# Optimization experiments

Measured on AMD Instinct MI355X. Metric: run time of the kernel, lower is better.

The kernel has to match this reference:

```python
import jax, jax.numpy as jnp
import numpy as np

N = 50000      # nodes
E = 800000     # unique directed edges (avg degree 16)
F = 64         # input_dim
D = 64         # output_dim (== F -> residual is identity)
ALPHA = 0.5
LCS_THR = 0.5  # enable_lcs_masking=True, lcs_threshold=0.5


def setup_inputs() -> dict:
    key = jax.random.key(0)
    ks = jax.random.split(key, 16)
    x = jax.random.normal(ks[0], (N, F), jnp.float32)
    src = jax.random.randint(ks[1], (E,), 0, N, jnp.int32)
    dst = jax.random.randint(ks[2], (E,), 0, N, jnp.int32)
    # integer-valued multiplicities in {1,2,3,4} (recurring-transaction counts)
    counts = jnp.floor(jax.random.uniform(ks[3], (E,), jnp.float32) * 4.0) + 1.0
    def lin(k, fan_in, shape):
        return jax.random.normal(k, shape, jnp.float32) / np.float32(np.sqrt(fan_in))
    return dict(
        x=x, counts=counts,
        W_s2d=lin(ks[4], F, (F, D)), b_s2d=jnp.zeros((D,), jnp.float32),
        W_d2s=lin(ks[5], F, (F, D)), b_d2s=jnp.zeros((D,), jnp.float32),
        W_l1=lin(ks[6], 2 * F, (2 * F, F)), b_l1=jnp.zeros((F,), jnp.float32),
        W_l2=lin(ks[7], F, (F, 1)), b_l2=jnp.zeros((1,), jnp.float32),
        W_g1=lin(ks[8], 2 * D, (2 * D, D)), b_g1=jnp.zeros((D,), jnp.float32),
        W_g2=lin(ks[9], D, (D, 1)), b_g2=jnp.zeros((1,), jnp.float32),
        src=src, dst=dst,
    )


def reference(x, counts, W_s2d, b_s2d, W_d2s, b_d2s,
              W_l1, b_l1, W_l2, b_l2, W_g1, b_g1, W_g2, b_g2,
              src, dst):
    # in/out degrees from full (unmasked) multiplicities, clamped at 1
    in_deg = jnp.maximum(jax.ops.segment_sum(counts, dst, num_segments=N), 1.0)
    out_deg = jnp.maximum(jax.ops.segment_sum(counts, src, num_segments=N), 1.0)

    # LCS per unique edge: sigmoid(MLP([x_src, x_dst])), detached in torch
    lcs_in = jnp.concatenate([x[src], x[dst]], axis=-1)          # [E, 2F]
    lcs = jax.nn.sigmoid(
        jax.nn.relu(lcs_in @ W_l1 + b_l1) @ W_l2 + b_l2)[:, 0]   # [E]
    lcs = jax.lax.stop_gradient(lcs)
    keep = (lcs >= LCS_THR).astype(x.dtype)                      # LCS masking

    # symmetric-normalized edge weights with multiplicity counts
    w = counts * keep * jax.lax.rsqrt(out_deg[src] * in_deg[dst])  # [E]

    # direction-aware message passing (redundancy-eliminated, per unique edge)
    h_s2d = x @ W_s2d + b_s2d                                    # [N, D]
    h_d2s = x @ W_d2s + b_d2s                                    # [N, D]
    m_in = jax.ops.segment_sum(w[:, None] * h_s2d[src], dst, num_segments=N)
    m_out = jax.ops.segment_sum(w[:, None] * h_d2s[dst], src, num_segments=N)

    # node-wise gating over inbound vs outbound flows
    gate = jax.nn.sigmoid(
        jax.nn.relu(jnp.concatenate([m_in, m_out], axis=-1) @ W_g1 + b_g1)
        @ W_g2 + b_g2)                                           # [N, 1]

    # gated alpha-blend + identity residual (input_dim == output_dim)
    out = ALPHA * gate * m_in + (1.0 - ALPHA) * (1.0 - gate) * m_out + x
    return out
```

## Files before the change

### kernel.cpp

```cpp
#include <hip/hip_runtime.h>
#include <math.h>


typedef unsigned long long u64;

#define SLOTS 56

__device__ __forceinline__ float bflo(unsigned u) { return __uint_as_float(u << 16); }
__device__ __forceinline__ float bfhi(unsigned u) { return __uint_as_float(u & 0xffff0000u); }
__device__ __forceinline__ unsigned rne16(float f) {
    unsigned u = __float_as_uint(f);
    return (u + 0x7fffu + ((u >> 16) & 1u)) >> 16;
}

__global__ __launch_bounds__(256, 2) void proj_zero_kernel(
    const float* __restrict__ x,
    const float* __restrict__ Wl1,  const float* __restrict__ bl1,
    const float* __restrict__ Ws2d, const float* __restrict__ bs2d,
    const float* __restrict__ Wd2s, const float* __restrict__ bd2s,
    const float* __restrict__ Wg1,  float* __restrict__ Wg1q,
    float* __restrict__ A, float* __restrict__ B,
    unsigned* __restrict__ Ah, unsigned* __restrict__ Bh,
    unsigned* __restrict__ HSh, unsigned* __restrict__ HDh,
    int4* __restrict__ zp4, int nz4, int PB, int N)
{
    if (blockIdx.x >= PB) {
        if (blockIdx.x == PB + 64) {
            for (int i = threadIdx.x; i < 8192; i += 256) {
                const int k = i >> 6, c = i & 63;
                Wg1q[((k >> 2) * 64 + c) * 4 + (k & 3)] = Wg1[i];
            }
            return;
        }
        const int t0 = (blockIdx.x - PB) * 256 + threadIdx.x;
        const int stride = 64 * 256;
        const int4 z = make_int4(0, 0, 0, 0);
        for (int i = t0; i < nz4; i += stride) zp4[i] = z;
        return;
    }
    __shared__ float xs[64][64];
    const int tid  = threadIdx.x;
    const int n0   = blockIdx.x * 64;
    const int wv   = tid >> 6;
    const int cc   = tid & 63;
    const int side = wv & 1;
    const int par  = wv >> 1;

    const float* W0 = side ? (Wl1 + 64 * 64) : Wl1;
    const float* W1 = side ? Wd2s : Ws2d;
    const float  b0 = side ? 0.f : bl1[cc];
    const float  b1 = side ? bd2s[cc] : bs2d[cc];
    float*    oA  = side ? B  : A;
    unsigned* oAh = side ? Bh : Ah;
    unsigned* oH  = side ? HDh : HSh;

    float w0[64], w1[64];
#pragma unroll
    for (int k = 0; k < 64; ++k) {
        w0[k] = W0[k * 64 + cc];
        w1[k] = W1[k * 64 + cc];
    }

#pragma unroll
    for (int j = 0; j < 4; ++j) {
        int f4  = tid + j * 256;
        int row = f4 >> 4;
        int c4  = f4 & 15;
        int gn  = n0 + row;
        float4 v = (gn < N) ? ((const float4*)x)[(long)gn * 16 + c4]
                            : make_float4(0.f, 0.f, 0.f, 0.f);
        ((float4*)&xs[row][0])[c4] = v;
    }
    __syncthreads();

    const int nmax = (N - n0 < 64) ? (N - n0) : 64;
    for (int n = par; n < nmax; n += 2) {
        float a0 = b0, a1 = b1;
#pragma unroll
        for (int k = 0; k < 64; k += 4) {
            float4 xv = *((const float4*)&xs[n][k]);
            a0 += xv.x * w0[k] + xv.y * w0[k + 1] + xv.z * w0[k + 2] + xv.w * w0[k + 3];
            a1 += xv.x * w1[k] + xv.y * w1[k + 1] + xv.z * w1[k + 2] + xv.w * w1[k + 3];
        }
        const long gn = n0 + n;
        oA[gn * 64 + cc] = a0;
        const float p0 = __shfl_xor(a0, 1);
        const float p1 = __shfl_xor(a1, 1);
        if ((cc & 1) == 0) {
            oAh[gn * 32 + (cc >> 1)] = (rne16(p0) << 16) | rne16(a0);
            oH [gn * 32 + (cc >> 1)] = (rne16(p1) << 16) | rne16(a1);
        }
    }
}

#define LCS_MARGIN 0.04f
__global__ __launch_bounds__(256) void edge_w_kernel(
    const int* __restrict__ src, const int* __restrict__ dst,
    const float* __restrict__ counts,
    const float* __restrict__ A, const float* __restrict__ B,
    const unsigned* __restrict__ Ah, const unsigned* __restrict__ Bh,
    const float* __restrict__ Wl2, const float* __restrict__ bl2,
    u64* __restrict__ pk, unsigned* __restrict__ rec, int N, int E)
{
    const int tid = threadIdx.x;
    const int e   = blockIdx.x * 32 + (tid >> 3);
    const int c   = tid & 7;
    if (e >= E) return;

    const int s = src[e];
    const int d = dst[e];
    const uint4  ua  = *((const uint4*)(Ah + (long)s * 32 + c * 4));
    const uint4  ub  = *((const uint4*)(Bh + (long)d * 32 + c * 4));
    const float4 wl0 = *((const float4*)(Wl2 + c * 8));
    const float4 wl1 = *((const float4*)(Wl2 + c * 8 + 4));

    float p = fmaxf(bflo(ua.x) + bflo(ub.x), 0.f) * wl0.x
            + fmaxf(bfhi(ua.x) + bfhi(ub.x), 0.f) * wl0.y
            + fmaxf(bflo(ua.y) + bflo(ub.y), 0.f) * wl0.z
            + fmaxf(bfhi(ua.y) + bfhi(ub.y), 0.f) * wl0.w
            + fmaxf(bflo(ua.z) + bflo(ub.z), 0.f) * wl1.x
            + fmaxf(bfhi(ua.z) + bfhi(ub.z), 0.f) * wl1.y
            + fmaxf(bflo(ua.w) + bflo(ub.w), 0.f) * wl1.z
            + fmaxf(bfhi(ua.w) + bfhi(ub.w), 0.f) * wl1.w;
    p += __shfl_xor(p, 1); p += __shfl_xor(p, 2); p += __shfl_xor(p, 4);

    float z = p + bl2[0];
    if (fabsf(z) < LCS_MARGIN) {
        const float4 a0 = *((const float4*)(A + (long)s * 64 + c * 8));
        const float4 a1 = *((const float4*)(A + (long)s * 64 + c * 8 + 4));
        const float4 b0 = *((const float4*)(B + (long)d * 64 + c * 8));
        const float4 b1 = *((const float4*)(B + (long)d * 64 + c * 8 + 4));
        float q = fmaxf(a0.x + b0.x, 0.f) * wl0.x + fmaxf(a0.y + b0.y, 0.f) * wl0.y
                + fmaxf(a0.z + b0.z, 0.f) * wl0.z + fmaxf(a0.w + b0.w, 0.f) * wl0.w
                + fmaxf(a1.x + b1.x, 0.f) * wl1.x + fmaxf(a1.y + b1.y, 0.f) * wl1.y
                + fmaxf(a1.z + b1.z, 0.f) * wl1.z + fmaxf(a1.w + b1.w, 0.f) * wl1.w;
        q += __shfl_xor(q, 1); q += __shfl_xor(q, 2); q += __shfl_xor(q, 4);
        z = q + bl2[0];
    }

    if (c == 0) {
        const u64 keep = (z >= 0.f) ? 1ull : 0ull;
        const unsigned ic = (unsigned)__float2int_rn(counts[e]);
        const u64 od = atomicAdd(pk + d,     (keep << 32) | (u64)ic);
        const u64 os = atomicAdd(pk + N + s, (keep << 32) | (u64)ic);
        if (keep) {
            rec[(long)d * SLOTS + (int)(od >> 32)]       = ((unsigned)s << 16) | ic;
            rec[(long)(N + s) * SLOTS + (int)(os >> 32)] = ((unsigned)d << 16) | ic;
        }
    }
}

__global__ __launch_bounds__(256) void gather_gate_kernel(
    const u64* __restrict__ pk, const unsigned* __restrict__ rec,
    const unsigned* __restrict__ HSh, const unsigned* __restrict__ HDh,
    const float* __restrict__ x,
    const float* __restrict__ Wg1q, const float* __restrict__ bg1,
    const float* __restrict__ Wg2, const float* __restrict__ bg2,
    float* __restrict__ out, int N)
{
    __shared__ float mbuf[16][128];
    const int tid  = threadIdx.x;
    const int wv   = tid >> 6;
    const int lane = tid & 63;
    const int g    = lane >> 3;
    const int c    = lane & 7;
    const int nb   = blockIdx.x * 16 + wv * 4;

    const unsigned* pklo = (const unsigned*)pk;

    for (int j = 0; j < 4; ++j) {
        const int n   = nb + j;
        const int row = wv * 4 + j;
        if (n >= N) {
            if (g == 0) {
#pragma unroll
                for (int q = 0; q < 8; ++q) {
                    mbuf[row][c * 8 + q]      = 0.f;
                    mbuf[row][64 + c * 8 + q] = 0.f;
                }
            }
            continue;
        }

        const u64 pin  = pk[n];
        const u64 pout = pk[N + n];
        const int ei = (int)(pin >> 32);
        const int eo = (int)(pout >> 32);
        const float qin  = 1.f / sqrtf(fmaxf((float)(unsigned)pin,  1.f));
        const float qout = 1.f / sqrtf(fmaxf((float)(unsigned)pout, 1.f));
        const unsigned* rin  = rec + (long)n * SLOTS;
        const unsigned* rout = rec + (long)(N + n) * SLOTS;

        float mi[8], mo[8];
#pragma unroll
        for (int q = 0; q < 8; ++q) { mi[q] = 0.f; mo[q] = 0.f; }

        int ii = g, jo = g;
        while ((ii < ei) || (jo < eo)) {
            const bool pa = ii < ei;
            const bool pb = jo < eo;
            const unsigned ra = rin[pa ? ii : 0];
            const unsigned rb = rout[pb ? jo : 0];
            const unsigned sa = ra >> 16;
            const unsigned sb = rb >> 16;
            const float dga = (float)pklo[2 * (N + (int)sa)];
            const float dgb = (float)pklo[2 * (int)sb];
            const float wa = pa ? (float)(ra & 0xFFu) * (1.f / sqrtf(fmaxf(dga, 1.f))) : 0.f;
            const float wb = pb ? (float)(rb & 0xFFu) * (1.f / sqrtf(fmaxf(dgb, 1.f))) : 0.f;
            const uint4 ua = *((const uint4*)(HSh + (long)sa * 32 + c * 4));
            const uint4 ub = *((const uint4*)(HDh + (long)sb * 32 + c * 4));
            mi[0] += wa * bflo(ua.x);  mo[0] += wb * bflo(ub.x);
            mi[1] += wa * bfhi(ua.x);  mo[1] += wb * bfhi(ub.x);
            mi[2] += wa * bflo(ua.y);  mo[2] += wb * bflo(ub.y);
            mi[3] += wa * bfhi(ua.y);  mo[3] += wb * bfhi(ub.y);
            mi[4] += wa * bflo(ua.z);  mo[4] += wb * bflo(ub.z);
            mi[5] += wa * bfhi(ua.z);  mo[5] += wb * bfhi(ub.z);
            mi[6] += wa * bflo(ua.w);  mo[6] += wb * bflo(ub.w);
            mi[7] += wa * bfhi(ua.w);  mo[7] += wb * bfhi(ub.w);
            ii += 8; jo += 8;
        }

#pragma unroll
        for (int q = 0; q < 8; ++q) {
            mi[q] += __shfl_xor(mi[q], 8);
            mi[q] += __shfl_xor(mi[q], 16);
            mi[q] += __shfl_xor(mi[q], 32);
            mo[q] += __shfl_xor(mo[q], 8);
            mo[q] += __shfl_xor(mo[q], 16);
            mo[q] += __shfl_xor(mo[q], 32);
        }
        if (g == 0) {
#pragma unroll
            for (int q = 0; q < 8; ++q) {
                mbuf[row][c * 8 + q]      = mi[q] * qin;
                mbuf[row][64 + c * 8 + q] = mo[q] * qout;
            }
        }
    }

    const float bgv = bg1[lane];
    float ac0 = bgv, ac1 = bgv, ac2 = bgv, ac3 = bgv;
    const float* m0 = &mbuf[wv * 4 + 0][0];
    const float* m1 = &mbuf[wv * 4 + 1][0];
    const float* m2 = &mbuf[wv * 4 + 2][0];
    const float* m3 = &mbuf[wv * 4 + 3][0];
#pragma unroll 4
    for (int k4 = 0; k4 < 32; ++k4) {
        const float4 w4 = ((const float4*)Wg1q)[k4 * 64 + lane];
        const float4 q0 = ((const float4*)m0)[k4];
        const float4 q1 = ((const float4*)m1)[k4];
        const float4 q2 = ((const float4*)m2)[k4];
        const float4 q3 = ((const float4*)m3)[k4];
        ac0 += q0.x * w4.x + q0.y * w4.y + q0.z * w4.z + q0.w * w4.w;
        ac1 += q1.x * w4.x + q1.y * w4.y + q1.z * w4.z + q1.w * w4.w;
        ac2 += q2.x * w4.x + q2.y * w4.y + q2.z * w4.z + q2.w * w4.w;
        ac3 += q3.x * w4.x + q3.y * w4.y + q3.z * w4.z + q3.w * w4.w;
    }
    const float wg2 = Wg2[lane];
    float v0 = fmaxf(ac0, 0.f) * wg2;
    float v1 = fmaxf(ac1, 0.f) * wg2;
    float v2 = fmaxf(ac2, 0.f) * wg2;
    float v3 = fmaxf(ac3, 0.f) * wg2;
#pragma unroll
    for (int m = 1; m <= 32; m <<= 1) {
        v0 += __shfl_xor(v0, m);
        v1 += __shfl_xor(v1, m);
        v2 += __shfl_xor(v2, m);
        v3 += __shfl_xor(v3, m);
    }
    const float bb = bg2[0];
    float gt[4];
    gt[0] = 1.f / (1.f + expf(-(v0 + bb)));
    gt[1] = 1.f / (1.f + expf(-(v1 + bb)));
    gt[2] = 1.f / (1.f + expf(-(v2 + bb)));
    gt[3] = 1.f / (1.f + expf(-(v3 + bb)));

#pragma unroll
    for (int j = 0; j < 4; ++j) {
        const int n = nb + j;
        if (n >= N) continue;
        const float miv = mbuf[wv * 4 + j][lane];
        const float mov = mbuf[wv * 4 + j][64 + lane];
        out[(long)n * 64 + lane] = 0.5f * gt[j] * miv + 0.5f * (1.f - gt[j]) * mov
                                 + x[(long)n * 64 + lane];
    }
}

extern "C" void kernel_launch(void* const* d_in, const int* in_sizes, int n_in,
                              void* d_out, int out_size, void* d_ws, size_t ws_size,
                              hipStream_t stream) {
    const float* x      = (const float*)d_in[0];
    const float* counts = (const float*)d_in[1];
    const float* Ws2d   = (const float*)d_in[2];
    const float* bs2d   = (const float*)d_in[3];
    const float* Wd2s   = (const float*)d_in[4];
    const float* bd2s   = (const float*)d_in[5];
    const float* Wl1    = (const float*)d_in[6];
    const float* bl1    = (const float*)d_in[7];
    const float* Wl2    = (const float*)d_in[8];
    const float* bl2    = (const float*)d_in[9];
    const float* Wg1    = (const float*)d_in[10];
    const float* bg1    = (const float*)d_in[11];
    const float* Wg2    = (const float*)d_in[12];
    const float* bg2    = (const float*)d_in[13];
    const int*   src    = (const int*)d_in[14];
    const int*   dst    = (const int*)d_in[15];

    const int N  = in_sizes[0] / 64;
    const int E  = in_sizes[14];
    const int PB = (N + 63) / 64;

    float* ws      = (float*)d_ws;
    float* Wg1q    = ws;
    float* A       = ws + 8192;
    float* B       = A + 64L * N;
    unsigned* Ah   = (unsigned*)(B + 64L * N);
    unsigned* Bh   = Ah + 32L * N;
    unsigned* HSh  = Bh + 32L * N;
    unsigned* HDh  = HSh + 32L * N;
    u64* pk        = (u64*)(HDh + 32L * N);
    unsigned* rec  = (unsigned*)(pk + 2L * N);

    proj_zero_kernel<<<PB + 65, 256, 0, stream>>>(
        x, Wl1, bl1, Ws2d, bs2d, Wd2s, bd2s, Wg1, Wg1q,
        A, B, Ah, Bh, HSh, HDh, (int4*)pk, N, PB, N);

    edge_w_kernel<<<(E + 31) / 32, 256, 0, stream>>>(
        src, dst, counts, A, B, Ah, Bh, Wl2, bl2, pk, rec, N, E);

    gather_gate_kernel<<<(N + 15) / 16, 256, 0, stream>>>(
        pk, rec, HSh, HDh, x, Wg1q, bg1, Wg2, bg2, (float*)d_out, N);
}
```

Measured before the change: 280.1 us.

## Split node projections across kernels to overlap H projection with edge work

The first kernel now computes only the LCS projections A/B (plus zeroing), with one weight column per thread instead of two, which cuts register pressure. It reads x directly from global memory instead of staging it in shared memory. The s2d/d2s H projections and the Wg1 repack move into extra blocks of the edge kernel so they can run alongside the per-edge LCS work. The trade-off is extra global reads of x and a heavier, mixed-role edge kernel launch.

```diff
diff --git a/kernel.cpp b/kernel.cpp
--- a/kernel.cpp
+++ b/kernel.cpp
@@ -13,98 +13,112 @@
     return (u + 0x7fffu + ((u >> 16) & 1u)) >> 16;
 }
 
-__global__ __launch_bounds__(256, 2) void proj_zero_kernel(
+__global__ __launch_bounds__(256) void projAB_zero_kernel(
     const float* __restrict__ x,
-    const float* __restrict__ Wl1,  const float* __restrict__ bl1,
-    const float* __restrict__ Ws2d, const float* __restrict__ bs2d,
-    const float* __restrict__ Wd2s, const float* __restrict__ bd2s,
-    const float* __restrict__ Wg1,  float* __restrict__ Wg1q,
+    const float* __restrict__ Wl1, const float* __restrict__ bl1,
     float* __restrict__ A, float* __restrict__ B,
     unsigned* __restrict__ Ah, unsigned* __restrict__ Bh,
-    unsigned* __restrict__ HSh, unsigned* __restrict__ HDh,
     int4* __restrict__ zp4, int nz4, int PB, int N)
 {
     if (blockIdx.x >= PB) {
-        if (blockIdx.x == PB + 64) {
-            for (int i = threadIdx.x; i < 8192; i += 256) {
-                const int k = i >> 6, c = i & 63;
-                Wg1q[((k >> 2) * 64 + c) * 4 + (k & 3)] = Wg1[i];
-            }
-            return;
-        }
         const int t0 = (blockIdx.x - PB) * 256 + threadIdx.x;
         const int stride = 64 * 256;
         const int4 z = make_int4(0, 0, 0, 0);
         for (int i = t0; i < nz4; i += stride) zp4[i] = z;
         return;
     }
-    __shared__ float xs[64][64];
     const int tid  = threadIdx.x;
     const int n0   = blockIdx.x * 64;
     const int wv   = tid >> 6;
     const int cc   = tid & 63;
     const int side = wv & 1;
-    const int par  = wv >> 1;
-
-    const float* W0 = side ? (Wl1 + 64 * 64) : Wl1;
-    const float* W1 = side ? Wd2s : Ws2d;
-    const float  b0 = side ? 0.f : bl1[cc];
-    const float  b1 = side ? bd2s[cc] : bs2d[cc];
+    const int par  = __builtin_amdgcn_readfirstlane(wv >> 1);
+
+    const float* W  = side ? (Wl1 + 64 * 64) : Wl1;
+    const float  bv = side ? 0.f : bl1[cc];
     float*    oA  = side ? B  : A;
     unsigned* oAh = side ? Bh : Ah;
-    unsigned* oH  = side ? HDh : HSh;
-
-    float w0[64], w1[64];
-#pragma unroll
-    for (int k = 0; k < 64; ++k) {
-        w0[k] = W0[k * 64 + cc];
-        w1[k] = W1[k * 64 + cc];
-    }
-
-#pragma unroll
-    for (int j = 0; j < 4; ++j) {
-        int f4  = tid + j * 256;
-        int row = f4 >> 4;
-        int c4  = f4 & 15;
-        int gn  = n0 + row;
-        float4 v = (gn < N) ? ((const float4*)x)[(long)gn * 16 + c4]
-                            : make_float4(0.f, 0.f, 0.f, 0.f);
-        ((float4*)&xs[row][0])[c4] = v;
-    }
-    __syncthreads();
+
+    float w[64];
+#pragma unroll
+    for (int k = 0; k < 64; ++k) w[k] = W[k * 64 + cc];
 
     const int nmax = (N - n0 < 64) ? (N - n0) : 64;
     for (int n = par; n < nmax; n += 2) {
-        float a0 = b0, a1 = b1;
-#pragma unroll
-        for (int k = 0; k < 64; k += 4) {
-            float4 xv = *((const float4*)&xs[n][k]);
-            a0 += xv.x * w0[k] + xv.y * w0[k + 1] + xv.z * w0[k + 2] + xv.w * w0[k + 3];
-            a1 += xv.x * w1[k] + xv.y * w1[k + 1] + xv.z * w1[k + 2] + xv.w * w1[k + 3];
+        const float* xr = x + (long)(n0 + n) * 64;
+        float acc = bv;
+#pragma unroll
+        for (int k4 = 0; k4 < 16; ++k4) {
+            const float4 xv = ((const float4*)xr)[k4];
+            acc += xv.x * w[4 * k4]     + xv.y * w[4 * k4 + 1]
+                 + xv.z * w[4 * k4 + 2] + xv.w * w[4 * k4 + 3];
         }
         const long gn = n0 + n;
-        oA[gn * 64 + cc] = a0;
-        const float p0 = __shfl_xor(a0, 1);
-        const float p1 = __shfl_xor(a1, 1);
-        if ((cc & 1) == 0) {
-            oAh[gn * 32 + (cc >> 1)] = (rne16(p0) << 16) | rne16(a0);
-            oH [gn * 32 + (cc >> 1)] = (rne16(p1) << 16) | rne16(a1);
-        }
+        oA[gn * 64 + cc] = acc;
+        const float p = __shfl_xor(acc, 1);
+        if ((cc & 1) == 0)
+            oAh[gn * 32 + (cc >> 1)] = (rne16(p) << 16) | rne16(acc);
     }
 }
 
 #define LCS_MARGIN 0.04f
-__global__ __launch_bounds__(256) void edge_w_kernel(
+__global__ __launch_bounds__(256) void edge_proj_kernel(
     const int* __restrict__ src, const int* __restrict__ dst,
     const float* __restrict__ counts,
     const float* __restrict__ A, const float* __restrict__ B,
     const unsigned* __restrict__ Ah, const unsigned* __restrict__ Bh,
     const float* __restrict__ Wl2, const float* __restrict__ bl2,
-    u64* __restrict__ pk, unsigned* __restrict__ rec, int N, int E)
+    u64* __restrict__ pk, unsigned* __restrict__ rec,
+    const float* __restrict__ x,
+    const float* __restrict__ Ws2d, const float* __restrict__ bs2d,
+    const float* __restrict__ Wd2s, const float* __restrict__ bd2s,
+    unsigned* __restrict__ HSh, unsigned* __restrict__ HDh,
+    const float* __restrict__ Wg1, float* __restrict__ Wg1q,
+    int PB, int N, int E)
 {
     const int tid = threadIdx.x;
-    const int e   = blockIdx.x * 32 + (tid >> 3);
-    const int c   = tid & 7;
+
+    if (blockIdx.x < PB) {
+        const int n0   = blockIdx.x * 64;
+        const int wv   = tid >> 6;
+        const int cc   = tid & 63;
+        const int side = wv & 1;
+        const int par  = __builtin_amdgcn_readfirstlane(wv >> 1);
+
+        const float* W  = side ? Wd2s : Ws2d;
+        const float  bv = side ? bd2s[cc] : bs2d[cc];
+        unsigned* oH = side ? HDh : HSh;
+
+        float w[64];
+#pragma unroll
+        for (int k = 0; k < 64; ++k) w[k] = W[k * 64 + cc];
+
+        const int nmax = (N - n0 < 64) ? (N - n0) : 64;
+        for (int n = par; n < nmax; n += 2) {
+            const float* xr = x + (long)(n0 + n) * 64;
+            float acc = bv;
+#pragma unroll
+            for (int k4 = 0; k4 < 16; ++k4) {
+                const float4 xv = ((const float4*)xr)[k4];
+                acc += xv.x * w[4 * k4]     + xv.y * w[4 * k4 + 1]
+                     + xv.z * w[4 * k4 + 2] + xv.w * w[4 * k4 + 3];
+            }
+            const float p = __shfl_xor(acc, 1);
+            if ((cc & 1) == 0)
+                oH[((long)(n0 + n)) * 32 + (cc >> 1)] = (rne16(p) << 16) | rne16(acc);
+        }
+        return;
+    }
+    if (blockIdx.x == PB) {
+        for (int i = tid; i < 8192; i += 256) {
+            const int k = i >> 6, c = i & 63;
+            Wg1q[((k >> 2) * 64 + c) * 4 + (k & 3)] = Wg1[i];
+        }
+        return;
+    }
+
+    const int e = (blockIdx.x - PB - 1) * 32 + (tid >> 3);
+    const int c = tid & 7;
     if (e >= E) return;
 
     const int s = src[e];
@@ -321,12 +335,12 @@
     u64* pk        = (u64*)(HDh + 32L * N);
     unsigned* rec  = (unsigned*)(pk + 2L * N);
 
-    proj_zero_kernel<<<PB + 65, 256, 0, stream>>>(
-        x, Wl1, bl1, Ws2d, bs2d, Wd2s, bd2s, Wg1, Wg1q,
-        A, B, Ah, Bh, HSh, HDh, (int4*)pk, N, PB, N);
-
-    edge_w_kernel<<<(E + 31) / 32, 256, 0, stream>>>(
-        src, dst, counts, A, B, Ah, Bh, Wl2, bl2, pk, rec, N, E);
+    projAB_zero_kernel<<<PB + 64, 256, 0, stream>>>(
+        x, Wl1, bl1, A, B, Ah, Bh, (int4*)pk, N, PB, N);
+
+    edge_proj_kernel<<<PB + 1 + (E + 31) / 32, 256, 0, stream>>>(
+        src, dst, counts, A, B, Ah, Bh, Wl2, bl2, pk, rec,
+        x, Ws2d, bs2d, Wd2s, bd2s, HSh, HDh, Wg1, Wg1q, PB, N, E);
 
     gather_gate_kernel<<<(N + 15) / 16, 256, 0, stream>>>(
         pk, rec, HSh, HDh, x, Wg1q, bg1, Wg2, bg2, (float*)d_out, N);
```

Result: slower. 292.0 us (+4.2%).
